# Kernel tuning notes

Hardware: AMD Instinct MI355X
Metric: run time of the kernel (lower is better)

The kernel has to match this reference:

```python
import jax, jax.numpy as jnp
import numpy as np

H = 16          # num_heads
R = 4           # query compression ratio
WIN = 128       # sliding window size
NEG = -1e9      # finite mask value (safe softmax grads)


def setup_inputs() -> dict:
    key = jax.random.key(0)
    k0, k1, k2, k3, k4 = jax.random.split(key, 5)
    B, S, D = 4, 4096, 2048
    inputs = jax.random.normal(k0, (B, S, D), jnp.float32)
    attention_mask = jnp.ones((B, S), jnp.int32)
    s = 0.02
    Wq = jax.random.normal(k1, (D, D), jnp.float32) * s
    Wk = jax.random.normal(k2, (D, D), jnp.float32) * s
    Wv = jax.random.normal(k3, (D, D), jnp.float32) * s
    Wo = jax.random.normal(k4, (D, D), jnp.float32) * s
    return {"inputs": inputs, "attention_mask": attention_mask,
            "Wq": Wq, "Wk": Wk, "Wv": Wv, "Wo": Wo}


def _forward(inputs, attention_mask, Wq, Wk, Wv, Wo):
    B, S, D = inputs.shape
    dh = D // H
    scale = 1.0 / np.sqrt(dh).astype(np.float32)
    Cs = (S + R - 1) // R            # compressed query length (S % R == 0 here)
    win = min(WIN, S)
    ws = max(0, S - win)             # window start

    # Q projection -> [B,H,S,dh] -> compress groups of R by mean -> [B,H,Cs,dh]
    q = jnp.einsum('bsd,od->bso', inputs, Wq)
    q = q.reshape(B, S, H, dh).transpose(0, 2, 1, 3)
    qc = q.reshape(B, H, Cs, R, dh).mean(axis=3)

    # K/V only over the recent window
    wx = inputs[:, ws:ws + win, :]
    k = jnp.einsum('bsd,od->bso', wx, Wk).reshape(B, win, H, dh).transpose(0, 2, 1, 3)
    v = jnp.einsum('bsd,od->bso', wx, Wv).reshape(B, win, H, dh).transpose(0, 2, 1, 3)

    scores = jnp.einsum('bhqd,bhkd->bhqk', qc, k) * scale

    # causal mask: each compressed query sits at position (i+1)*R-1
    qpos = (jnp.arange(Cs) + 1) * R - 1                     # [Cs]
    wpos = ws + jnp.arange(win)
    causal = wpos[None, :] <= qpos[:, None]
    qbw = qpos < ws                                         # queries fully before window
    causal = causal.at[:, 0].set(causal[:, 0] | qbw)
    pad_ok = (attention_mask[:, ws:ws + win] != 0)
    full = causal[None, None, :, :] & pad_ok[:, None, None, :]

    scores = jnp.where(full, scores, NEG)
    weights = jax.nn.softmax(scores, axis=-1)
    out = jnp.einsum('bhqk,bhkd->bhqd', weights, v)         # [B,H,Cs,dh]
    out = out.transpose(0, 2, 1, 3).reshape(B, Cs, D)
    out = jnp.einsum('bsd,od->bso', out, Wo)

    if Cs != S:  # linear interpolation back to seq_len (align_corners=False)
        out = jax.image.resize(out, (B, S, D), method='linear')
    return out


def reference(inputs, attention_mask, Wq, Wk, Wv, Wo):
    return _forward(inputs, attention_mask, Wq, Wk, Wv, Wo)
```

## Files before the change

### kernel.cpp

```cpp
#include <hip/hip_runtime.h>
#include <hip/hip_bf16.h>


typedef __attribute__((ext_vector_type(8))) short short8;
typedef __attribute__((ext_vector_type(4))) float f32x4;

#define QP_SLICE  (128 * 2048)
#define KV_SLICE  (512 * 2048)
#define YO_STRIDE (132 * 2048)

__device__ __forceinline__ unsigned short f2bf(float f){
  unsigned int x = __float_as_uint(f);
  return (unsigned short)((x + 0x7fffu + ((x >> 16) & 1u)) >> 16);
}
__device__ __forceinline__ float bf2f(unsigned short u){
  return __uint_as_float(((unsigned int)u) << 16);
}
__device__ __forceinline__ float bflo(unsigned int u){ return __uint_as_float(u << 16); }
__device__ __forceinline__ float bfhi(unsigned int u){ return __uint_as_float(u & 0xffff0000u); }
__device__ __forceinline__ unsigned int pk2(float lo, float hi){
  return ((unsigned int)f2bf(hi) << 16) | (unsigned int)f2bf(lo);
}
__device__ __forceinline__ short8 cvt8(float4 x, float4 y){
  union { unsigned int u[4]; short8 s; } r;
  r.u[0] = pk2(x.x, x.y); r.u[1] = pk2(x.z, x.w);
  r.u[2] = pk2(y.x, y.y); r.u[3] = pk2(y.z, y.w);
  return r.s;
}

__global__ __launch_bounds__(256) void prep_kernel(
    const float* __restrict__ inp,
    const float* __restrict__ Wq, const float* __restrict__ Wk,
    const float* __restrict__ Wv, const float* __restrict__ Wo,
    unsigned short* __restrict__ Wb,
    unsigned short* __restrict__ Awx, unsigned short* __restrict__ Aq)
{
  const int bx = blockIdx.x;
  if (bx < 8192){
    const int idx = bx * 256 + threadIdx.x;
    const int w = idx >> 19;
    const int sub = idx & 524287;
    const float* src = (w == 0) ? Wq : (w == 1) ? Wk : (w == 2) ? Wv : Wo;
    const float* p = src + (size_t)sub * 8;
    *(short8*)&Wb[(size_t)w * 4194304 + (size_t)sub * 8] =
        cvt8(*(const float4*)p, *(const float4*)(p + 4));
  } else if (bx < 8704){
    const int idx = (bx - 8192) * 256 + threadIdx.x;
    const int b = idx >> 15;
    const int j = (idx >> 8) & 127;
    const int d8 = (idx & 255) * 8;
    const float* p = inp + ((size_t)b * 4096 + 3968 + j) * 2048 + d8;
    *(short8*)&Awx[((size_t)b * 128 + j) * 2048 + d8] =
        cvt8(*(const float4*)p, *(const float4*)(p + 4));
  } else {
    const int idx = (bx - 8704) * 256 + threadIdx.x;
    const int b = idx >> 13;
    const int c = (idx >> 8) & 31;
    const int d8 = (idx & 255) * 8;
    const float* p = inp + ((size_t)b * 4096 + 3968 + 4 * c) * 2048 + d8;
    float4 x0 = *(const float4*)(p);
    float4 x1 = *(const float4*)(p + 2048);
    float4 x2 = *(const float4*)(p + 4096);
    float4 x3 = *(const float4*)(p + 6144);
    float4 y0 = *(const float4*)(p + 4);
    float4 y1 = *(const float4*)(p + 2052);
    float4 y2 = *(const float4*)(p + 4100);
    float4 y3 = *(const float4*)(p + 6148);
    float4 xm, ym;
    xm.x = 0.25f * (x0.x + x1.x + x2.x + x3.x);
    xm.y = 0.25f * (x0.y + x1.y + x2.y + x3.y);
    xm.z = 0.25f * (x0.z + x1.z + x2.z + x3.z);
    xm.w = 0.25f * (x0.w + x1.w + x2.w + x3.w);
    ym.x = 0.25f * (y0.x + y1.x + y2.x + y3.x);
    ym.y = 0.25f * (y0.y + y1.y + y2.y + y3.y);
    ym.z = 0.25f * (y0.z + y1.z + y2.z + y3.z);
    ym.w = 0.25f * (y0.w + y1.w + y2.w + y3.w);
    *(short8*)&Aq[((size_t)b * 32 + c) * 2048 + d8] = cvt8(xm, ym);
  }
}

__device__ __forceinline__ void stage_tile(
    const unsigned short* __restrict__ A, const unsigned short* __restrict__ W,
    int row0, int n0, int kt,
    unsigned short* As, unsigned short* Bs, int wid, int lane)
{
  const int r = lane >> 3, u = (lane & 7) * 8;
  #pragma unroll
  for (int i = 0; i < 4; ++i){
    const int c = wid * 4 + i;
    __builtin_amdgcn_global_load_lds(
        (const __attribute__((address_space(1))) void*)(A + (size_t)(row0 + c * 8 + r) * 2048 + kt + u),
        (__attribute__((address_space(3))) void*)(As + c * 512),
        16, 0, 0);
    __builtin_amdgcn_global_load_lds(
        (const __attribute__((address_space(1))) void*)(W + (size_t)(n0 + c * 8 + r) * 2048 + kt + u),
        (__attribute__((address_space(3))) void*)(Bs + c * 512),
        16, 0, 0);
  }
}

template<bool OUT_BF16>
__device__ __forceinline__ void gemm_body(
    const unsigned short* __restrict__ A, const unsigned short* __restrict__ W,
    unsigned short* __restrict__ Cb, float* __restrict__ Cf,
    int M, int row0, int n0, int kbase, int nsteps,
    unsigned short* L)
{
  const int tid  = threadIdx.x;
  const int lane = tid & 63;
  const int wid  = tid >> 6;
  const int wr = wid >> 1, wc = wid & 1;

  f32x4 acc[4][4] = {};

  stage_tile(A, W, row0, n0, kbase, L, L + 8192, wid, lane);
  int cur = 0;

  for (int t = 0; t < nsteps; ++t){
    __syncthreads();
    const int nxt = cur ^ 1;
    if (t + 1 < nsteps)
      stage_tile(A, W, row0, n0, kbase + (t + 1) * 64,
                 L + nxt * 16384, L + nxt * 16384 + 8192, wid, lane);
    const unsigned short* As = L + cur * 16384;
    const unsigned short* Bs = As + 8192;
    #pragma unroll
    for (int ks = 0; ks < 2; ++ks){
      short8 av[4], bv[4];
      #pragma unroll
      for (int f = 0; f < 4; ++f)
        av[f] = *(const short8*)&As[(wr * 64 + f * 16 + (lane & 15)) * 64 + ks * 32 + (lane >> 4) * 8];
      #pragma unroll
      for (int n = 0; n < 4; ++n)
        bv[n] = *(const short8*)&Bs[(wc * 64 + n * 16 + (lane & 15)) * 64 + ks * 32 + (lane >> 4) * 8];
      #pragma unroll
      for (int f = 0; f < 4; ++f)
        #pragma unroll
        for (int n = 0; n < 4; ++n)
          acc[f][n] = __builtin_amdgcn_mfma_f32_16x16x32_bf16(av[f], bv[n], acc[f][n], 0, 0, 0);
    }
    cur = nxt;
  }

  #pragma unroll
  for (int f = 0; f < 4; ++f){
    #pragma unroll
    for (int n = 0; n < 4; ++n){
      const int col = n0 + wc * 64 + n * 16 + (lane & 15);
      #pragma unroll
      for (int r = 0; r < 4; ++r){
        const int row = row0 + wr * 64 + f * 16 + (lane >> 4) * 4 + r;
        if (row < M){
          if (OUT_BF16) Cb[(size_t)row * 2048 + col] = f2bf(acc[f][n][r]);
          else          Cf[(size_t)row * 2048 + col] = acc[f][n][r];
        }
      }
    }
  }
}

__global__ __launch_bounds__(256, 2) void qkv_kernel(
    const unsigned short* __restrict__ Aq, const unsigned short* __restrict__ Awx,
    const unsigned short* __restrict__ Wb,
    unsigned short* __restrict__ Qp, unsigned short* __restrict__ Kp,
    unsigned short* __restrict__ Vp)
{
  __shared__ __align__(16) unsigned short L[4 * 16384 / 2];
  const int nt = blockIdx.x, gy = blockIdx.y;
  if (gy < 4){
    gemm_body<true>(Aq, Wb, Qp + gy * QP_SLICE, nullptr,
                    128, 0, nt * 128, gy * 512, 8, L);
  } else if (gy < 20){
    const int idx = gy - 4, mt = idx >> 2, ksp = idx & 3;
    gemm_body<true>(Awx, Wb + 4194304, Kp + ksp * KV_SLICE, nullptr,
                    512, mt * 128, nt * 128, ksp * 512, 8, L);
  } else {
    const int idx = gy - 20, mt = idx >> 2, ksp = idx & 3;
    gemm_body<true>(Awx, Wb + 8388608, Vp + ksp * KV_SLICE, nullptr,
                    512, mt * 128, nt * 128, ksp * 512, 8, L);
  }
}

__global__ __launch_bounds__(256, 2) void o_kernel(
    const unsigned short* __restrict__ Ao, const unsigned short* __restrict__ Wb,
    float* __restrict__ Yop)
{
  __shared__ __align__(16) unsigned short L[32768];
  gemm_body<false>(Ao, Wb + 12582912, nullptr, Yop + (size_t)blockIdx.z * YO_STRIDE,
                   132, blockIdx.y * 128, blockIdx.x * 128, blockIdx.z * 512, 8, L);
}

__global__ __launch_bounds__(256) void attn_kernel(
    const unsigned short* __restrict__ Qp, const unsigned short* __restrict__ Kp,
    const unsigned short* __restrict__ Vp, const int* __restrict__ amask,
    unsigned short* __restrict__ Ao)
{
  const int b = blockIdx.x >> 4;
  const int h = blockIdx.x & 15;
  __shared__ float Qs[32][129];
  __shared__ unsigned int Ks[128][65];
  __shared__ unsigned int Vs[128][65];
  __shared__ float Wt[32][132];
  __shared__ float msk[128];
  const int tid = threadIdx.x;

  for (int i = tid; i < 32 * 128; i += 256){
    int cq = i >> 7, d = i & 127;
    size_t off = (size_t)(b * 32 + cq) * 2048 + h * 128 + d;
    Qs[cq][d] = bf2f(Qp[off]) + bf2f(Qp[off + QP_SLICE]) +
                bf2f(Qp[off + 2 * QP_SLICE]) + bf2f(Qp[off + 3 * QP_SLICE]);
  }
  for (int i = tid; i < 128 * 64; i += 256){
    int j = i >> 6, du = i & 63;
    size_t off = (size_t)(b * 128 + j) * 2048 + h * 128 + du * 2;
    unsigned int k0 = *(const unsigned int*)(Kp + off);
    unsigned int k1 = *(const unsigned int*)(Kp + off + KV_SLICE);
    unsigned int k2 = *(const unsigned int*)(Kp + off + 2 * KV_SLICE);
    unsigned int k3 = *(const unsigned int*)(Kp + off + 3 * KV_SLICE);
    unsigned int v0 = *(const unsigned int*)(Vp + off);
    unsigned int v1 = *(const unsigned int*)(Vp + off + KV_SLICE);
    unsigned int v2 = *(const unsigned int*)(Vp + off + 2 * KV_SLICE);
    unsigned int v3 = *(const unsigned int*)(Vp + off + 3 * KV_SLICE);
    Ks[j][du] = pk2(bflo(k0) + bflo(k1) + bflo(k2) + bflo(k3),
                    bfhi(k0) + bfhi(k1) + bfhi(k2) + bfhi(k3));
    Vs[j][du] = pk2(bflo(v0) + bflo(v1) + bflo(v2) + bflo(v3),
                    bfhi(v0) + bfhi(v1) + bfhi(v2) + bfhi(v3));
  }
  if (tid < 128){
    msk[tid] = (amask[b * 4096 + 3968 + tid] != 0) ? 1.f : 0.f;
    size_t off = (size_t)(b * 128) * 2048 + h * 128 + tid;
    Ao[(size_t)(b * 33) * 2048 + h * 128 + tid] =
        f2bf(bf2f(Vp[off]) + bf2f(Vp[off + KV_SLICE]) +
             bf2f(Vp[off + 2 * KV_SLICE]) + bf2f(Vp[off + 3 * KV_SLICE]));
  }
  __syncthreads();

  const int cq = tid >> 3, jg = tid & 7;
  const int jmax = 4 * cq + 3;
  const float scale = 0.088388347648318447f;

  float s[16];
  {
    float sacc[16];
    #pragma unroll
    for (int jj = 0; jj < 16; ++jj) sacc[jj] = 0.f;
    for (int du = 0; du < 64; ++du){
      float q0 = Qs[cq][2 * du], q1 = Qs[cq][2 * du + 1];
      #pragma unroll
      for (int jj = 0; jj < 16; ++jj){
        unsigned int u = Ks[jg * 16 + jj][du];
        sacc[jj] += q0 * bflo(u) + q1 * bfhi(u);
      }
    }
    #pragma unroll
    for (int jj = 0; jj < 16; ++jj){
      int j = jg * 16 + jj;
      bool ok = (j <= jmax) && (msk[j] > 0.5f);
      s[jj] = ok ? sacc[jj] * scale : -1e9f;
    }
  }
  float m = s[0];
  #pragma unroll
  for (int jj = 1; jj < 16; ++jj) m = fmaxf(m, s[jj]);
  #pragma unroll
  for (int off = 1; off < 8; off <<= 1) m = fmaxf(m, __shfl_xor(m, off, 8));
  float sum = 0.f;
  #pragma unroll
  for (int jj = 0; jj < 16; ++jj){ s[jj] = expf(s[jj] - m); sum += s[jj]; }
  #pragma unroll
  for (int off = 1; off < 8; off <<= 1) sum += __shfl_xor(sum, off, 8);
  const float inv = 1.f / sum;
  #pragma unroll
  for (int jj = 0; jj < 16; ++jj) Wt[cq][jg * 16 + jj] = s[jj] * inv;
  __syncthreads();

  const int dg = tid & 7;
  float o[16];
  #pragma unroll
  for (int e = 0; e < 16; ++e) o[e] = 0.f;
  for (int j = 0; j < 128; ++j){
    float w = Wt[cq][j];
    #pragma unroll
    for (int du = 0; du < 8; ++du){
      unsigned int u = Vs[j][dg * 8 + du];
      o[2 * du]     += w * bflo(u);
      o[2 * du + 1] += w * bfhi(u);
    }
  }
  unsigned short* dst = Ao + (size_t)(b * 33 + 1 + cq) * 2048 + h * 128 + dg * 16;
  #pragma unroll
  for (int e = 0; e < 16; ++e) dst[e] = f2bf(o[e]);
}

__global__ __launch_bounds__(256) void resize_kernel(
    const float* __restrict__ Yop, float* __restrict__ out)
{
  const int rowid = blockIdx.x;
  const int b = rowid >> 12;
  const int i = rowid & 4095;
  float c  = i * 0.25f - 0.375f;
  float fl = floorf(c);
  int   j0 = (int)fl;
  float f  = c - fl;
  int   j1 = j0 + 1;
  j0 = max(0, min(j0, 1023));
  j1 = max(0, min(j1, 1023));
  const int ri0 = b * 33 + (j0 <= 991 ? 0 : j0 - 991);
  const int ri1 = b * 33 + (j1 <= 991 ? 0 : j1 - 991);
  const float* r0 = Yop + (size_t)ri0 * 2048;
  const float* r1 = Yop + (size_t)ri1 * 2048;
  float* op = out + (size_t)rowid * 2048;
  const int t = threadIdx.x;
  const bool same = (ri0 == ri1);
  #pragma unroll
  for (int q = 0; q < 2; ++q){
    int d = q * 1024 + t * 4;
    float4 a0 = *(const float4*)(r0 + d);
    float4 a1 = *(const float4*)(r0 + d + YO_STRIDE);
    float4 a2 = *(const float4*)(r0 + d + 2 * YO_STRIDE);
    float4 a3 = *(const float4*)(r0 + d + 3 * YO_STRIDE);
    float4 a;
    a.x = a0.x + a1.x + a2.x + a3.x;
    a.y = a0.y + a1.y + a2.y + a3.y;
    a.z = a0.z + a1.z + a2.z + a3.z;
    a.w = a0.w + a1.w + a2.w + a3.w;
    float4 o = a;
    if (!same){
      float4 b0 = *(const float4*)(r1 + d);
      float4 b1 = *(const float4*)(r1 + d + YO_STRIDE);
      float4 b2 = *(const float4*)(r1 + d + 2 * YO_STRIDE);
      float4 b3 = *(const float4*)(r1 + d + 3 * YO_STRIDE);
      float4 bb;
      bb.x = b0.x + b1.x + b2.x + b3.x;
      bb.y = b0.y + b1.y + b2.y + b3.y;
      bb.z = b0.z + b1.z + b2.z + b3.z;
      bb.w = b0.w + b1.w + b2.w + b3.w;
      o.x = a.x + f * (bb.x - a.x);
      o.y = a.y + f * (bb.y - a.y);
      o.z = a.z + f * (bb.z - a.z);
      o.w = a.w + f * (bb.w - a.w);
    }
    *(float4*)(op + d) = o;
  }
}

extern "C" void kernel_launch(void* const* d_in, const int* in_sizes, int n_in,
                              void* d_out, int out_size, void* d_ws, size_t ws_size,
                              hipStream_t stream)
{
  const float* inp   = (const float*)d_in[0];
  const int*   amask = (const int*)d_in[1];
  const float* Wq = (const float*)d_in[2];
  const float* Wk = (const float*)d_in[3];
  const float* Wv = (const float*)d_in[4];
  const float* Wo = (const float*)d_in[5];
  float* out = (float*)d_out;

  char* ws = (char*)d_ws;
  unsigned short* Wb  = (unsigned short*)(ws);
  unsigned short* Aq  = (unsigned short*)(ws + 33554432);
  unsigned short* Awx = (unsigned short*)(ws + 34078720);
  unsigned short* Qp  = (unsigned short*)(ws + 36175872);
  unsigned short* Kp  = (unsigned short*)(ws + 38273024);
  unsigned short* Vp  = (unsigned short*)(ws + 46661632);
  unsigned short* Ao  = (unsigned short*)(ws + 55050240);
  float*          Yop = (float*)(ws + 56623104);

  prep_kernel<<<8832, 256, 0, stream>>>(inp, Wq, Wk, Wv, Wo, Wb, Awx, Aq);
  qkv_kernel<<<dim3(16, 36), 256, 0, stream>>>(Aq, Awx, Wb, Qp, Kp, Vp);
  attn_kernel<<<64, 256, 0, stream>>>(Qp, Kp, Vp, amask, Ao);
  o_kernel<<<dim3(16, 2, 4), 256, 0, stream>>>(Ao, Wb, Yop);
  resize_kernel<<<16384, 256, 0, stream>>>(Yop, out);
}
```

Before: 118.1 us.

## Fuse QKV, attention and O-projection into persistent kernel with grid barriers

Replaces three separate launches (QKV GEMM, attention, O GEMM) with one persistent kernel of 512 blocks that loops over the QKV tiles and uses atomic global barriers between stages, removing launch gaps. It also XOR-swizzles the LDS layout of GEMM tiles to reduce bank conflicts, stores Q as packed bf16 in shared memory, and restructures the attention PV product so each thread reduces over its own weights with shuffle reductions instead of staging weights in LDS. The grid barrier depends on all 512 blocks being co-resident and adds spin-wait overhead. 576 QKV tiles over 512 blocks leaves a tail where a few blocks do two tiles, and large shared memory may limit occupancy.

```diff
diff --git a/kernel.cpp b/kernel.cpp
--- a/kernel.cpp
+++ b/kernel.cpp
@@ -5,6 +5,7 @@
 typedef __attribute__((ext_vector_type(8))) short short8;
 typedef __attribute__((ext_vector_type(4))) float f32x4;
 
+#define NBLOCKS 512
 #define QP_SLICE  (128 * 2048)
 #define KV_SLICE  (512 * 2048)
 #define YO_STRIDE (132 * 2048)
@@ -26,6 +27,24 @@
   r.u[0] = pk2(x.x, x.y); r.u[1] = pk2(x.z, x.w);
   r.u[2] = pk2(y.x, y.y); r.u[3] = pk2(y.z, y.w);
   return r.s;
+}
+
+__device__ __forceinline__ void gsync(unsigned int* cnt, unsigned int* gen){
+  __syncthreads();
+  if (threadIdx.x == 0){
+    unsigned int g = __hip_atomic_load(gen, __ATOMIC_RELAXED, __HIP_MEMORY_SCOPE_AGENT);
+    __threadfence();
+    unsigned int a = __hip_atomic_fetch_add(cnt, 1u, __ATOMIC_ACQ_REL, __HIP_MEMORY_SCOPE_AGENT);
+    if (a == NBLOCKS - 1){
+      __hip_atomic_store(cnt, 0u, __ATOMIC_RELAXED, __HIP_MEMORY_SCOPE_AGENT);
+      __hip_atomic_fetch_add(gen, 1u, __ATOMIC_ACQ_REL, __HIP_MEMORY_SCOPE_AGENT);
+    } else {
+      while (__hip_atomic_load(gen, __ATOMIC_ACQUIRE, __HIP_MEMORY_SCOPE_AGENT) == g)
+        __builtin_amdgcn_s_sleep(8);
+    }
+    __threadfence();
+  }
+  __syncthreads();
 }
 
 __global__ __launch_bounds__(256) void prep_kernel(
@@ -84,16 +103,17 @@
     int row0, int n0, int kt,
     unsigned short* As, unsigned short* Bs, int wid, int lane)
 {
-  const int r = lane >> 3, u = (lane & 7) * 8;
+  const int r  = lane >> 3;
+  const int ug = ((lane & 7) ^ r) * 8;
   #pragma unroll
   for (int i = 0; i < 4; ++i){
     const int c = wid * 4 + i;
     __builtin_amdgcn_global_load_lds(
-        (const __attribute__((address_space(1))) void*)(A + (size_t)(row0 + c * 8 + r) * 2048 + kt + u),
+        (const __attribute__((address_space(1))) void*)(A + (size_t)(row0 + c * 8 + r) * 2048 + kt + ug),
         (__attribute__((address_space(3))) void*)(As + c * 512),
         16, 0, 0);
     __builtin_amdgcn_global_load_lds(
-        (const __attribute__((address_space(1))) void*)(W + (size_t)(n0 + c * 8 + r) * 2048 + kt + u),
+        (const __attribute__((address_space(1))) void*)(W + (size_t)(n0 + c * 8 + r) * 2048 + kt + ug),
         (__attribute__((address_space(3))) void*)(Bs + c * 512),
         16, 0, 0);
   }
@@ -127,12 +147,17 @@
     #pragma unroll
     for (int ks = 0; ks < 2; ++ks){
       short8 av[4], bv[4];
-      #pragma unroll
-      for (int f = 0; f < 4; ++f)
-        av[f] = *(const short8*)&As[(wr * 64 + f * 16 + (lane & 15)) * 64 + ks * 32 + (lane >> 4) * 8];
-      #pragma unroll
-      for (int n = 0; n < 4; ++n)
-        bv[n] = *(const short8*)&Bs[(wc * 64 + n * 16 + (lane & 15)) * 64 + ks * 32 + (lane >> 4) * 8];
+      const int unit = ks * 4 + (lane >> 4);
+      #pragma unroll
+      for (int f = 0; f < 4; ++f){
+        const int row = wr * 64 + f * 16 + (lane & 15);
+        av[f] = *(const short8*)&As[row * 64 + ((unit ^ (row & 7)) * 8)];
+      }
+      #pragma unroll
+      for (int n = 0; n < 4; ++n){
+        const int row = wc * 64 + n * 16 + (lane & 15);
+        bv[n] = *(const short8*)&Bs[row * 64 + ((unit ^ (row & 7)) * 8)];
+      }
       #pragma unroll
       for (int f = 0; f < 4; ++f)
         #pragma unroll
@@ -159,79 +184,49 @@
   }
 }
 
-__global__ __launch_bounds__(256, 2) void qkv_kernel(
-    const unsigned short* __restrict__ Aq, const unsigned short* __restrict__ Awx,
-    const unsigned short* __restrict__ Wb,
-    unsigned short* __restrict__ Qp, unsigned short* __restrict__ Kp,
-    unsigned short* __restrict__ Vp)
-{
-  __shared__ __align__(16) unsigned short L[4 * 16384 / 2];
-  const int nt = blockIdx.x, gy = blockIdx.y;
-  if (gy < 4){
-    gemm_body<true>(Aq, Wb, Qp + gy * QP_SLICE, nullptr,
-                    128, 0, nt * 128, gy * 512, 8, L);
-  } else if (gy < 20){
-    const int idx = gy - 4, mt = idx >> 2, ksp = idx & 3;
-    gemm_body<true>(Awx, Wb + 4194304, Kp + ksp * KV_SLICE, nullptr,
-                    512, mt * 128, nt * 128, ksp * 512, 8, L);
-  } else {
-    const int idx = gy - 20, mt = idx >> 2, ksp = idx & 3;
-    gemm_body<true>(Awx, Wb + 8388608, Vp + ksp * KV_SLICE, nullptr,
-                    512, mt * 128, nt * 128, ksp * 512, 8, L);
-  }
-}
-
-__global__ __launch_bounds__(256, 2) void o_kernel(
-    const unsigned short* __restrict__ Ao, const unsigned short* __restrict__ Wb,
-    float* __restrict__ Yop)
-{
-  __shared__ __align__(16) unsigned short L[32768];
-  gemm_body<false>(Ao, Wb + 12582912, nullptr, Yop + (size_t)blockIdx.z * YO_STRIDE,
-                   132, blockIdx.y * 128, blockIdx.x * 128, blockIdx.z * 512, 8, L);
-}
-
-__global__ __launch_bounds__(256) void attn_kernel(
+__device__ void attn_body(
     const unsigned short* __restrict__ Qp, const unsigned short* __restrict__ Kp,
     const unsigned short* __restrict__ Vp, const int* __restrict__ amask,
-    unsigned short* __restrict__ Ao)
-{
-  const int b = blockIdx.x >> 4;
-  const int h = blockIdx.x & 15;
-  __shared__ float Qs[32][129];
-  __shared__ unsigned int Ks[128][65];
-  __shared__ unsigned int Vs[128][65];
-  __shared__ float Wt[32][132];
-  __shared__ float msk[128];
+    unsigned short* __restrict__ Ao, char* smem, int b, int h)
+{
+  unsigned int (*Ks)[65] = (unsigned int(*)[65])smem;
+  unsigned int (*Vs)[65] = (unsigned int(*)[65])(smem + 33280);
+  unsigned int (*Qs)[65] = (unsigned int(*)[65])(smem + 66560);
+  float* msk = (float*)(smem + 74880);
   const int tid = threadIdx.x;
 
-  for (int i = tid; i < 32 * 128; i += 256){
-    int cq = i >> 7, d = i & 127;
-    size_t off = (size_t)(b * 32 + cq) * 2048 + h * 128 + d;
-    Qs[cq][d] = bf2f(Qp[off]) + bf2f(Qp[off + QP_SLICE]) +
-                bf2f(Qp[off + 2 * QP_SLICE]) + bf2f(Qp[off + 3 * QP_SLICE]);
+  for (int i = tid; i < 32 * 64; i += 256){
+    int cq = i >> 6, du = i & 63;
+    size_t off = (size_t)(b * 32 + cq) * 2048 + h * 128 + du * 2;
+    float lo = 0.f, hi = 0.f;
+    #pragma unroll
+    for (int s4 = 0; s4 < 4; ++s4){
+      unsigned int q = *(const unsigned int*)(Qp + off + (size_t)s4 * QP_SLICE);
+      lo += bflo(q); hi += bfhi(q);
+    }
+    Qs[cq][du] = pk2(lo, hi);
   }
   for (int i = tid; i < 128 * 64; i += 256){
     int j = i >> 6, du = i & 63;
     size_t off = (size_t)(b * 128 + j) * 2048 + h * 128 + du * 2;
-    unsigned int k0 = *(const unsigned int*)(Kp + off);
-    unsigned int k1 = *(const unsigned int*)(Kp + off + KV_SLICE);
-    unsigned int k2 = *(const unsigned int*)(Kp + off + 2 * KV_SLICE);
-    unsigned int k3 = *(const unsigned int*)(Kp + off + 3 * KV_SLICE);
-    unsigned int v0 = *(const unsigned int*)(Vp + off);
-    unsigned int v1 = *(const unsigned int*)(Vp + off + KV_SLICE);
-    unsigned int v2 = *(const unsigned int*)(Vp + off + 2 * KV_SLICE);
-    unsigned int v3 = *(const unsigned int*)(Vp + off + 3 * KV_SLICE);
-    Ks[j][du] = pk2(bflo(k0) + bflo(k1) + bflo(k2) + bflo(k3),
-                    bfhi(k0) + bfhi(k1) + bfhi(k2) + bfhi(k3));
-    Vs[j][du] = pk2(bflo(v0) + bflo(v1) + bflo(v2) + bflo(v3),
-                    bfhi(v0) + bfhi(v1) + bfhi(v2) + bfhi(v3));
+    float klo = 0.f, khi = 0.f, vlo = 0.f, vhi = 0.f;
+    #pragma unroll
+    for (int s4 = 0; s4 < 4; ++s4){
+      unsigned int k = *(const unsigned int*)(Kp + off + (size_t)s4 * KV_SLICE);
+      unsigned int v = *(const unsigned int*)(Vp + off + (size_t)s4 * KV_SLICE);
+      klo += bflo(k); khi += bfhi(k);
+      vlo += bflo(v); vhi += bfhi(v);
+    }
+    Ks[j][du] = pk2(klo, khi);
+    Vs[j][du] = pk2(vlo, vhi);
   }
   if (tid < 128){
     msk[tid] = (amask[b * 4096 + 3968 + tid] != 0) ? 1.f : 0.f;
     size_t off = (size_t)(b * 128) * 2048 + h * 128 + tid;
-    Ao[(size_t)(b * 33) * 2048 + h * 128 + tid] =
-        f2bf(bf2f(Vp[off]) + bf2f(Vp[off + KV_SLICE]) +
-             bf2f(Vp[off + 2 * KV_SLICE]) + bf2f(Vp[off + 3 * KV_SLICE]));
+    float v = 0.f;
+    #pragma unroll
+    for (int s4 = 0; s4 < 4; ++s4) v += bf2f(Vp[off + (size_t)s4 * KV_SLICE]);
+    Ao[(size_t)(b * 33) * 2048 + h * 128 + tid] = f2bf(v);
   }
   __syncthreads();
 
@@ -245,7 +240,8 @@
     #pragma unroll
     for (int jj = 0; jj < 16; ++jj) sacc[jj] = 0.f;
     for (int du = 0; du < 64; ++du){
-      float q0 = Qs[cq][2 * du], q1 = Qs[cq][2 * du + 1];
+      unsigned int qq = Qs[cq][du];
+      float q0 = bflo(qq), q1 = bfhi(qq);
       #pragma unroll
       for (int jj = 0; jj < 16; ++jj){
         unsigned int u = Ks[jg * 16 + jj][du];
@@ -271,25 +267,76 @@
   for (int off = 1; off < 8; off <<= 1) sum += __shfl_xor(sum, off, 8);
   const float inv = 1.f / sum;
   #pragma unroll
-  for (int jj = 0; jj < 16; ++jj) Wt[cq][jg * 16 + jj] = s[jj] * inv;
-  __syncthreads();
-
-  const int dg = tid & 7;
-  float o[16];
-  #pragma unroll
-  for (int e = 0; e < 16; ++e) o[e] = 0.f;
-  for (int j = 0; j < 128; ++j){
-    float w = Wt[cq][j];
-    #pragma unroll
-    for (int du = 0; du < 8; ++du){
-      unsigned int u = Vs[j][dg * 8 + du];
-      o[2 * du]     += w * bflo(u);
-      o[2 * du + 1] += w * bfhi(u);
-    }
-  }
-  unsigned short* dst = Ao + (size_t)(b * 33 + 1 + cq) * 2048 + h * 128 + dg * 16;
-  #pragma unroll
-  for (int e = 0; e < 16; ++e) dst[e] = f2bf(o[e]);
+  for (int jj = 0; jj < 16; ++jj) s[jj] *= inv;
+
+  #pragma unroll
+  for (int db = 0; db < 8; ++db){
+    float o[16];
+    #pragma unroll
+    for (int e = 0; e < 16; ++e) o[e] = 0.f;
+    #pragma unroll
+    for (int jj = 0; jj < 16; ++jj){
+      const float w = s[jj];
+      const int j = jg * 16 + jj;
+      #pragma unroll
+      for (int du2 = 0; du2 < 8; ++du2){
+        unsigned int u = Vs[j][db * 8 + du2];
+        o[2 * du2]     += w * bflo(u);
+        o[2 * du2 + 1] += w * bfhi(u);
+      }
+    }
+    #pragma unroll
+    for (int e = 0; e < 16; ++e){
+      o[e] += __shfl_xor(o[e], 1, 8);
+      o[e] += __shfl_xor(o[e], 2, 8);
+      o[e] += __shfl_xor(o[e], 4, 8);
+    }
+    if (jg == db){
+      unsigned short* dst = Ao + (size_t)(b * 33 + 1 + cq) * 2048 + h * 128 + db * 16;
+      #pragma unroll
+      for (int e = 0; e < 16; ++e) dst[e] = f2bf(o[e]);
+    }
+  }
+}
+
+__global__ __launch_bounds__(256, 2) void mega_kernel(
+    const unsigned short* __restrict__ Aq, const unsigned short* __restrict__ Awx,
+    const unsigned short* __restrict__ Wb,
+    unsigned short* __restrict__ Qp, unsigned short* __restrict__ Kp,
+    unsigned short* __restrict__ Vp,
+    const int* __restrict__ amask, unsigned short* __restrict__ Ao,
+    float* __restrict__ Yop, unsigned int* __restrict__ bar)
+{
+  __shared__ __align__(16) char smem[75392];
+  unsigned short* L = (unsigned short*)smem;
+  const int bid = blockIdx.x;
+
+  for (int t = bid; t < 576; t += NBLOCKS){
+    const int nt = t & 15, gy = t >> 4;
+    if (gy < 4){
+      gemm_body<true>(Aq, Wb, Qp + gy * QP_SLICE, nullptr,
+                      128, 0, nt * 128, gy * 512, 8, L);
+    } else if (gy < 20){
+      const int idx = gy - 4, mt = idx >> 2, ksp = idx & 3;
+      gemm_body<true>(Awx, Wb + 4194304, Kp + ksp * KV_SLICE, nullptr,
+                      512, mt * 128, nt * 128, ksp * 512, 8, L);
+    } else {
+      const int idx = gy - 20, mt = idx >> 2, ksp = idx & 3;
+      gemm_body<true>(Awx, Wb + 8388608, Vp + ksp * KV_SLICE, nullptr,
+                      512, mt * 128, nt * 128, ksp * 512, 8, L);
+    }
+    __syncthreads();
+  }
+  gsync(bar, bar + 1);
+
+  if (bid < 64) attn_body(Qp, Kp, Vp, amask, Ao, smem, bid >> 4, bid & 15);
+  gsync(bar, bar + 1);
+
+  if (bid < 128){
+    const int nt = bid & 15, mt = (bid >> 4) & 1, ksp = bid >> 5;
+    gemm_body<false>(Ao, Wb + 12582912, nullptr, Yop + (size_t)ksp * YO_STRIDE,
+                     132, mt * 128, nt * 128, ksp * 512, 8, L);
+  }
 }
 
 __global__ __launch_bounds__(256) void resize_kernel(
@@ -365,10 +412,10 @@
   unsigned short* Vp  = (unsigned short*)(ws + 46661632);
   unsigned short* Ao  = (unsigned short*)(ws + 55050240);
   float*          Yop = (float*)(ws + 56623104);
-
+  unsigned int*   bar = (unsigned int*)(ws + 60948480);
+
+  hipMemsetAsync(bar, 0, 8, stream);
   prep_kernel<<<8832, 256, 0, stream>>>(inp, Wq, Wk, Wv, Wo, Wb, Awx, Aq);
-  qkv_kernel<<<dim3(16, 36), 256, 0, stream>>>(Aq, Awx, Wb, Qp, Kp, Vp);
-  attn_kernel<<<64, 256, 0, stream>>>(Qp, Kp, Vp, amask, Ao);
-  o_kernel<<<dim3(16, 2, 4), 256, 0, stream>>>(Ao, Wb, Yop);
+  mega_kernel<<<NBLOCKS, 256, 0, stream>>>(Aq, Awx, Wb, Qp, Kp, Vp, amask, Ao, Yop, bar);
   resize_kernel<<<16384, 256, 0, stream>>>(Yop, out);
 }
```

After: 358.1 us. +203.2%, slower.
